# Kernel optimization log

Measured on AMD Instinct MI355X. Metric: run time of the kernel, lower is better.

## Reference

```python
import jax, jax.numpy as jnp
import numpy as np
import math

NUM_LANDMARKS = 64
HEAD_DIM = 64
NUM_HEAD = 16
BATCH = 4
SEQ_LEN = 4096


def iterative_inv(mat, n_iter=6):
    # mat: [..., m, m]
    I = jnp.eye(mat.shape[-1], dtype=mat.dtype)
    K = mat
    # scalar normalization: global max of column sums * global max of row sums
    scale = 1.0 / (jnp.max(jnp.sum(jnp.abs(K), axis=-2)) * jnp.max(jnp.sum(jnp.abs(K), axis=-1)))
    V = scale * jnp.swapaxes(K, -1, -2)
    for _ in range(n_iter):
        KV = jnp.matmul(K, V)
        V = jnp.matmul(0.25 * V, 13.0 * I - jnp.matmul(KV, 15.0 * I - jnp.matmul(KV, 7.0 * I - KV)))
    return V


def setup_inputs() -> dict:
    key = jax.random.key(0)
    k1, k2, k3 = jax.random.split(key, 3)
    shape = (BATCH, NUM_HEAD, SEQ_LEN, HEAD_DIM)
    Q = jax.random.normal(k1, shape, dtype=jnp.float32)
    K = jax.random.normal(k2, shape, dtype=jnp.float32)
    V = jax.random.normal(k3, shape, dtype=jnp.float32)
    return {"Q": Q, "K": K, "V": V}


def reference(Q, K, V):
    seq_len = Q.shape[-2]
    m = NUM_LANDMARKS
    scale = 1.0 / math.sqrt(math.sqrt(HEAD_DIM))
    Q = Q * scale
    K = K * scale
    # landmark pooling: mean over contiguous segments of length seq_len // m
    seg = seq_len // m
    Q_lm = Q.reshape(-1, NUM_HEAD, m, seg, HEAD_DIM).mean(axis=-2)  # [B,H,m,d]
    K_lm = K.reshape(-1, NUM_HEAD, m, seg, HEAD_DIM).mean(axis=-2)  # [B,H,m,d]
    # three softmax kernels
    kernel_1 = jax.nn.softmax(jnp.einsum('bhsd,bhmd->bhsm', Q, K_lm), axis=-1)   # [B,H,S,m]
    kernel_2 = jax.nn.softmax(jnp.einsum('bhmd,bhnd->bhmn', Q_lm, K_lm), axis=-1)  # [B,H,m,m]
    kernel_3 = jax.nn.softmax(jnp.einsum('bhmd,bhsd->bhms', Q_lm, K), axis=-1)   # [B,H,m,S]
    inv_k2 = iterative_inv(kernel_2)
    X = jnp.matmul(jnp.matmul(kernel_1, inv_k2), jnp.matmul(kernel_3, V))  # [B,H,S,d]
    return X
```

## Files before the change

### kernel.cpp

```cpp
#include <hip/hip_runtime.h>
#include <hip/hip_bf16.h>

#define PAD 68
#define KP  72
#define SCALE 0.35355339059327379f

typedef __attribute__((ext_vector_type(8))) short bf16x8;
typedef __attribute__((ext_vector_type(4))) float f32x4;
#define MFMA_BF16 __builtin_amdgcn_mfma_f32_16x16x32_bf16

__device__ __forceinline__ short f2b(float f) {
    unsigned u = __float_as_uint(f);
    u += 0x7fff + ((u >> 16) & 1);
    return (short)(u >> 16);
}
__device__ __forceinline__ float b2f(short h) {
    return __uint_as_float(((unsigned)(unsigned short)h) << 16);
}

__device__ __forceinline__ void fma16(float acc[16], float a, const float* b) {
    const float4* b4 = reinterpret_cast<const float4*>(b);
    float4 x0 = b4[0], x1 = b4[1], x2 = b4[2], x3 = b4[3];
    acc[0]  += a * x0.x; acc[1]  += a * x0.y; acc[2]  += a * x0.z; acc[3]  += a * x0.w;
    acc[4]  += a * x1.x; acc[5]  += a * x1.y; acc[6]  += a * x1.z; acc[7]  += a * x1.w;
    acc[8]  += a * x2.x; acc[9]  += a * x2.y; acc[10] += a * x2.z; acc[11] += a * x2.w;
    acc[12] += a * x3.x; acc[13] += a * x3.y; acc[14] += a * x3.z; acc[15] += a * x3.w;
}

__device__ __forceinline__ void mm_tile(float acc[4][4],
                                        const float* __restrict__ A, int lda,
                                        const float* __restrict__ B,
                                        int i0, int j0) {
#pragma unroll
    for (int r = 0; r < 4; r++)
#pragma unroll
        for (int c = 0; c < 4; c++) acc[r][c] = 0.f;
#pragma unroll 4
    for (int k0 = 0; k0 < 64; k0 += 4) {
        float4 b0 = *reinterpret_cast<const float4*>(&B[(k0 + 0) * PAD + j0]);
        float4 b1 = *reinterpret_cast<const float4*>(&B[(k0 + 1) * PAD + j0]);
        float4 b2 = *reinterpret_cast<const float4*>(&B[(k0 + 2) * PAD + j0]);
        float4 b3 = *reinterpret_cast<const float4*>(&B[(k0 + 3) * PAD + j0]);
        float4 a0 = *reinterpret_cast<const float4*>(&A[(i0 + 0) * lda + k0]);
        float4 a1 = *reinterpret_cast<const float4*>(&A[(i0 + 1) * lda + k0]);
        float4 a2 = *reinterpret_cast<const float4*>(&A[(i0 + 2) * lda + k0]);
        float4 a3 = *reinterpret_cast<const float4*>(&A[(i0 + 3) * lda + k0]);
#define ROW_UPD(r, av) \
        acc[r][0] += av.x * b0.x + av.y * b1.x + av.z * b2.x + av.w * b3.x; \
        acc[r][1] += av.x * b0.y + av.y * b1.y + av.z * b2.y + av.w * b3.y; \
        acc[r][2] += av.x * b0.z + av.y * b1.z + av.z * b2.z + av.w * b3.z; \
        acc[r][3] += av.x * b0.w + av.y * b1.w + av.z * b2.w + av.w * b3.w;
        ROW_UPD(0, a0) ROW_UPD(1, a1) ROW_UPD(2, a2) ROW_UPD(3, a3)
#undef ROW_UPD
    }
}

__global__ __launch_bounds__(256) void pool_kernel(const float* __restrict__ Q,
                                                   const float* __restrict__ K,
                                                   float* __restrict__ Qlm,
                                                   float* __restrict__ Klm) {
    __shared__ float4 red[256];
    const int blk = blockIdx.x;
    const int t = threadIdx.x;
    const int d4 = t & 15;
    const int rg = t >> 4;
    const float4* Q4 = reinterpret_cast<const float4*>(Q);
    const float4* K4 = reinterpret_cast<const float4*>(K);

    float4 sQ = {0.f, 0.f, 0.f, 0.f}, sK = {0.f, 0.f, 0.f, 0.f};
#pragma unroll
    for (int rr = 0; rr < 4; rr++) {
        int row = blk * 64 + rg * 4 + rr;
        int off4 = (row << 4) + d4;
        float4 q = Q4[off4], k = K4[off4];
        sQ.x += q.x; sQ.y += q.y; sQ.z += q.z; sQ.w += q.w;
        sK.x += k.x; sK.y += k.y; sK.z += k.z; sK.w += k.w;
    }
    const float c = SCALE * (1.0f / 64.0f);
    red[t] = sQ;
    __syncthreads();
    if (t < 16) {
        float4 s = {0.f, 0.f, 0.f, 0.f};
#pragma unroll
        for (int g = 0; g < 16; g++) {
            float4 v = red[g * 16 + t];
            s.x += v.x; s.y += v.y; s.z += v.z; s.w += v.w;
        }
        s.x *= c; s.y *= c; s.z *= c; s.w *= c;
        reinterpret_cast<float4*>(Qlm + blk * 64)[t] = s;
    }
    __syncthreads();
    red[t] = sK;
    __syncthreads();
    if (t < 16) {
        float4 s = {0.f, 0.f, 0.f, 0.f};
#pragma unroll
        for (int g = 0; g < 16; g++) {
            float4 v = red[g * 16 + t];
            s.x += v.x; s.y += v.y; s.z += v.z; s.w += v.w;
        }
        s.x *= c; s.y *= c; s.z *= c; s.w *= c;
        reinterpret_cast<float4*>(Klm + blk * 64)[t] = s;
    }
}

__global__ __launch_bounds__(256) void k2_kernel(const float* __restrict__ Qlm,
                                                 const float* __restrict__ Klm,
                                                 float* __restrict__ K2g,
                                                 unsigned* __restrict__ colmax) {
    __shared__ float Ql[64 * PAD], Kl[64 * PAD], S2[64 * PAD];
    const int bh = blockIdx.x, t = threadIdx.x;
#pragma unroll
    for (int n = 0; n < 16; n++) {
        int f = t + n * 256;
        Ql[(f >> 6) * PAD + (f & 63)] = Qlm[bh * 4096 + f];
        Kl[(f >> 6) * PAD + (f & 63)] = Klm[bh * 4096 + f];
    }
    __syncthreads();
    const int i = t >> 2, j0 = (t & 3) * 16;
    float acc[16];
#pragma unroll
    for (int u = 0; u < 16; u++) acc[u] = 0.f;
    const float4* Ql4 = reinterpret_cast<const float4*>(Ql);
    const float4* Kl4 = reinterpret_cast<const float4*>(Kl);
    for (int k4 = 0; k4 < 16; k4++) {
        float4 a = Ql4[i * 17 + k4];
#pragma unroll
        for (int u = 0; u < 16; u++) {
            float4 b = Kl4[(j0 + u) * 17 + k4];
            acc[u] += a.x * b.x + a.y * b.y + a.z * b.z + a.w * b.w;
        }
    }
#pragma unroll
    for (int u = 0; u < 16; u++) S2[i * PAD + j0 + u] = acc[u];
    __syncthreads();
    if (t < 64) {
        float m = -1e30f;
        for (int j = 0; j < 64; j++) m = fmaxf(m, S2[t * PAD + j]);
        float sum = 0.f;
        for (int j = 0; j < 64; j++) {
            float e = __expf(S2[t * PAD + j] - m);
            S2[t * PAD + j] = e; sum += e;
        }
        float inv = 1.0f / sum;
        for (int j = 0; j < 64; j++) S2[t * PAD + j] *= inv;
    }
    __syncthreads();
#pragma unroll
    for (int n = 0; n < 16; n++) {
        int f = t + n * 256;
        K2g[bh * 4096 + f] = S2[(f >> 6) * PAD + (f & 63)];
    }
    if (t < 64) {
        float c = 0.f;
        for (int ii = 0; ii < 64; ii++) c += S2[ii * PAD + t];
        atomicMax(colmax, __float_as_uint(c));
    }
}

__global__ __launch_bounds__(256) void fused_inv_k3v(const float* __restrict__ Qlm,
                                                     const float* __restrict__ K,
                                                     const float* __restrict__ V,
                                                     float* __restrict__ W2acc,
                                                     float* __restrict__ rowsum3,
                                                     const float* __restrict__ K2g,
                                                     const unsigned* __restrict__ colmax,
                                                     float* __restrict__ K2invg) {
    __shared__ __align__(16) char smem[64 * PAD * 4 * 3];
    const int t = threadIdx.x;

    if (blockIdx.x < 64) {
        float* Vb = reinterpret_cast<float*>(smem);
        float* Ab = Vb + 64 * PAD;
        float* Tb = Ab + 64 * PAD;
        const int bh = blockIdx.x;
        const float sc = 1.0f / __uint_as_float(*colmax);
        const float* Kg = K2g + bh * 4096;
#pragma unroll
        for (int n = 0; n < 16; n++) {
            int f = t + n * 256;
            Vb[(f >> 6) * PAD + (f & 63)] = sc * Kg[(f & 63) * 64 + (f >> 6)];
        }
        __syncthreads();
        const int i0 = (t >> 4) * 4, j0 = (t & 15) * 4;
        float acc[4][4], vacc[4][4];
        for (int iter = 0; iter < 6; iter++) {
            mm_tile(acc, Kg, 64, Vb, i0, j0);
#pragma unroll
            for (int r = 0; r < 4; r++)
                *reinterpret_cast<float4*>(&Ab[(i0 + r) * PAD + j0]) =
                    make_float4(acc[r][0], acc[r][1], acc[r][2], acc[r][3]);
            __syncthreads();
            mm_tile(acc, Vb, PAD, Ab, i0, j0);
#pragma unroll
            for (int r = 0; r < 4; r++) {
                float4 v = *reinterpret_cast<const float4*>(&Vb[(i0 + r) * PAD + j0]);
                vacc[r][0] = 13.f * v.x - 15.f * acc[r][0];
                vacc[r][1] = 13.f * v.y - 15.f * acc[r][1];
                vacc[r][2] = 13.f * v.z - 15.f * acc[r][2];
                vacc[r][3] = 13.f * v.w - 15.f * acc[r][3];
                *reinterpret_cast<float4*>(&Tb[(i0 + r) * PAD + j0]) =
                    make_float4(acc[r][0], acc[r][1], acc[r][2], acc[r][3]);
            }
            __syncthreads();
            mm_tile(acc, Tb, PAD, Ab, i0, j0);
#pragma unroll
            for (int r = 0; r < 4; r++) {
                vacc[r][0] += 7.f * acc[r][0];
                vacc[r][1] += 7.f * acc[r][1];
                vacc[r][2] += 7.f * acc[r][2];
                vacc[r][3] += 7.f * acc[r][3];
                *reinterpret_cast<float4*>(&Vb[(i0 + r) * PAD + j0]) =
                    make_float4(acc[r][0], acc[r][1], acc[r][2], acc[r][3]);
            }
            __syncthreads();
            mm_tile(acc, Vb, PAD, Ab, i0, j0);
#pragma unroll
            for (int r = 0; r < 4; r++) {
                vacc[r][0] -= acc[r][0]; vacc[r][1] -= acc[r][1];
                vacc[r][2] -= acc[r][2]; vacc[r][3] -= acc[r][3];
            }
            __syncthreads();
#pragma unroll
            for (int r = 0; r < 4; r++)
                *reinterpret_cast<float4*>(&Vb[(i0 + r) * PAD + j0]) =
                    make_float4(0.25f * vacc[r][0], 0.25f * vacc[r][1],
                                0.25f * vacc[r][2], 0.25f * vacc[r][3]);
            __syncthreads();
        }
#pragma unroll
        for (int n = 0; n < 16; n++) {
            int f = t + n * 256;
            K2invg[bh * 4096 + f] = Vb[(f >> 6) * PAD + (f & 63)];
        }
        return;
    }

    short* Qs = reinterpret_cast<short*>(smem);
    short* Kt = Qs + 64 * KP;
    short* Vt = Kt + 64 * KP;
    short* Eb = Vt + 64 * KP;
    const int idx = blockIdx.x - 64;
    const int chunk = idx & 15, bh = idx >> 4;
    const int w = t >> 6, lane = t & 63, quad = lane >> 4, l15 = lane & 15;
    const float4* Qlm4 = reinterpret_cast<const float4*>(Qlm);
    const float4* K4 = reinterpret_cast<const float4*>(K);
    const float4* V4 = reinterpret_cast<const float4*>(V);

#pragma unroll
    for (int n = 0; n < 4; n++) {
        int f4 = t + n * 256;
        int r = f4 >> 4, dg = f4 & 15;
        float4 q = Qlm4[bh * 1024 + f4];
        ushort4 uq = { (unsigned short)f2b(q.x), (unsigned short)f2b(q.y),
                       (unsigned short)f2b(q.z), (unsigned short)f2b(q.w) };
        *reinterpret_cast<ushort4*>(&Qs[r * KP + dg * 4]) = uq;
    }

    f32x4 oacc[4];
    float rsum[4];
#pragma unroll
    for (int nt = 0; nt < 4; nt++) { oacc[nt] = (f32x4){0.f, 0.f, 0.f, 0.f}; rsum[nt] = 0.f; }

    for (int tile = 0; tile < 4; tile++) {
        const int sb = chunk * 256 + tile * 64;
        __syncthreads();
#pragma unroll
        for (int n = 0; n < 4; n++) {
            int f4 = t + n * 256;
            int key = f4 >> 4, dg = f4 & 15;
            int g4 = (bh * 4096 + sb + key) * 16 + dg;
            float4 kk = K4[g4];
            ushort4 uk = { (unsigned short)f2b(SCALE * kk.x), (unsigned short)f2b(SCALE * kk.y),
                           (unsigned short)f2b(SCALE * kk.z), (unsigned short)f2b(SCALE * kk.w) };
            *reinterpret_cast<ushort4*>(&Kt[key * KP + dg * 4]) = uk;
            float4 vv = V4[g4];
            Vt[(dg * 4 + 0) * KP + key] = f2b(vv.x);
            Vt[(dg * 4 + 1) * KP + key] = f2b(vv.y);
            Vt[(dg * 4 + 2) * KP + key] = f2b(vv.z);
            Vt[(dg * 4 + 3) * KP + key] = f2b(vv.w);
        }
        __syncthreads();
        bf16x8 a0 = *reinterpret_cast<const bf16x8*>(&Qs[(w * 16 + l15) * KP + quad * 8]);
        bf16x8 a1 = *reinterpret_cast<const bf16x8*>(&Qs[(w * 16 + l15) * KP + quad * 8 + 32]);
#pragma unroll
        for (int nt = 0; nt < 4; nt++) {
            bf16x8 b0 = *reinterpret_cast<const bf16x8*>(&Kt[(nt * 16 + l15) * KP + quad * 8]);
            bf16x8 b1 = *reinterpret_cast<const bf16x8*>(&Kt[(nt * 16 + l15) * KP + quad * 8 + 32]);
            f32x4 c = {0.f, 0.f, 0.f, 0.f};
            c = MFMA_BF16(a0, b0, c, 0, 0, 0);
            c = MFMA_BF16(a1, b1, c, 0, 0, 0);
#pragma unroll
            for (int reg = 0; reg < 4; reg++) {
                float e = __expf(c[reg]);
                rsum[reg] += e;
                Eb[(w * 16 + quad * 4 + reg) * KP + nt * 16 + l15] = f2b(e);
            }
        }
        bf16x8 e0 = *reinterpret_cast<const bf16x8*>(&Eb[(w * 16 + l15) * KP + quad * 8]);
        bf16x8 e1 = *reinterpret_cast<const bf16x8*>(&Eb[(w * 16 + l15) * KP + quad * 8 + 32]);
#pragma unroll
        for (int nt = 0; nt < 4; nt++) {
            bf16x8 b0 = *reinterpret_cast<const bf16x8*>(&Vt[(nt * 16 + l15) * KP + quad * 8]);
            bf16x8 b1 = *reinterpret_cast<const bf16x8*>(&Vt[(nt * 16 + l15) * KP + quad * 8 + 32]);
            oacc[nt] = MFMA_BF16(e0, b0, oacc[nt], 0, 0, 0);
            oacc[nt] = MFMA_BF16(e1, b1, oacc[nt], 0, 0, 0);
        }
    }
#pragma unroll
    for (int reg = 0; reg < 4; reg++) {
        float s = rsum[reg];
        s += __shfl_xor(s, 1); s += __shfl_xor(s, 2);
        s += __shfl_xor(s, 4); s += __shfl_xor(s, 8);
        rsum[reg] = s;
    }
    const int row0 = w * 16 + quad * 4;
    if (l15 == 0) {
#pragma unroll
        for (int reg = 0; reg < 4; reg++)
            atomicAdd(&rowsum3[bh * 64 + row0 + reg], rsum[reg]);
    }
#pragma unroll
    for (int nt = 0; nt < 4; nt++)
#pragma unroll
        for (int reg = 0; reg < 4; reg++)
            atomicAdd(&W2acc[(bh * 64 + row0 + reg) * 64 + nt * 16 + l15], oacc[nt][reg]);
}

__global__ __launch_bounds__(256) void wmid_kernel(const float* __restrict__ K2invg,
                                                   const float* __restrict__ W2acc,
                                                   const float* __restrict__ rowsum3,
                                                   float* __restrict__ Wg) {
    __shared__ float I1[64 * PAD], W2[64 * PAD];
    const int bh = blockIdx.x, t = threadIdx.x;
#pragma unroll
    for (int n = 0; n < 16; n++) {
        int f = t + n * 256;
        int r = f >> 6;
        I1[r * PAD + (f & 63)] = K2invg[bh * 4096 + f];
        W2[r * PAD + (f & 63)] = W2acc[bh * 4096 + f] / rowsum3[bh * 64 + r];
    }
    __syncthreads();
    const int i = t >> 2, j0 = (t & 3) * 16;
    float acc[16];
#pragma unroll
    for (int u = 0; u < 16; u++) acc[u] = 0.f;
    for (int k = 0; k < 64; k++) fma16(acc, I1[i * PAD + k], W2 + k * PAD + j0);
#pragma unroll
    for (int u = 0; u < 16; u++) Wg[bh * 4096 + i * 64 + j0 + u] = acc[u];
}

__global__ __launch_bounds__(256) void final_mfma(const float* __restrict__ Q,
                                                  const float* __restrict__ Klm,
                                                  const float* __restrict__ Wg,
                                                  float* __restrict__ out) {
    __shared__ short Qs[64 * KP];
    __shared__ short Kl[64 * KP];
    __shared__ short Eb[64 * KP];
    __shared__ short Wh[64 * KP];
    __shared__ short Wl[64 * KP];
    const int sc = blockIdx.x, bh = blockIdx.y, t = threadIdx.x;
    const int w = t >> 6, lane = t & 63, quad = lane >> 4, l15 = lane & 15;
    const int s0 = sc * 64;
    const float4* Q4 = reinterpret_cast<const float4*>(Q);
    const float4* Klm4 = reinterpret_cast<const float4*>(Klm);
    const float4* W4 = reinterpret_cast<const float4*>(Wg);

#pragma unroll
    for (int n = 0; n < 4; n++) {
        int f4 = t + n * 256;
        int r = f4 >> 4, dg = f4 & 15;
        float4 kl = Klm4[bh * 1024 + f4];
        ushort4 uk = { (unsigned short)f2b(kl.x), (unsigned short)f2b(kl.y),
                       (unsigned short)f2b(kl.z), (unsigned short)f2b(kl.w) };
        *reinterpret_cast<ushort4*>(&Kl[r * KP + dg * 4]) = uk;
        float4 q = Q4[(bh * 4096 + s0 + r) * 16 + dg];
        ushort4 uq = { (unsigned short)f2b(SCALE * q.x), (unsigned short)f2b(SCALE * q.y),
                       (unsigned short)f2b(SCALE * q.z), (unsigned short)f2b(SCALE * q.w) };
        *reinterpret_cast<ushort4*>(&Qs[r * KP + dg * 4]) = uq;
        float4 ww = W4[bh * 1024 + f4];
        float wv[4] = {ww.x, ww.y, ww.z, ww.w};
#pragma unroll
        for (int i = 0; i < 4; i++) {
            short hi = f2b(wv[i]);
            Wh[(dg * 4 + i) * KP + r] = hi;
            Wl[(dg * 4 + i) * KP + r] = f2b(wv[i] - b2f(hi));
        }
    }
    __syncthreads();
    bf16x8 a0 = *reinterpret_cast<const bf16x8*>(&Qs[(w * 16 + l15) * KP + quad * 8]);
    bf16x8 a1 = *reinterpret_cast<const bf16x8*>(&Qs[(w * 16 + l15) * KP + quad * 8 + 32]);
    float rsum[4] = {0.f, 0.f, 0.f, 0.f};
#pragma unroll
    for (int nt = 0; nt < 4; nt++) {
        bf16x8 b0 = *reinterpret_cast<const bf16x8*>(&Kl[(nt * 16 + l15) * KP + quad * 8]);
        bf16x8 b1 = *reinterpret_cast<const bf16x8*>(&Kl[(nt * 16 + l15) * KP + quad * 8 + 32]);
        f32x4 c = {0.f, 0.f, 0.f, 0.f};
        c = MFMA_BF16(a0, b0, c, 0, 0, 0);
        c = MFMA_BF16(a1, b1, c, 0, 0, 0);
#pragma unroll
        for (int reg = 0; reg < 4; reg++) {
            float e = __expf(c[reg]);
            rsum[reg] += e;
            Eb[(w * 16 + quad * 4 + reg) * KP + nt * 16 + l15] = f2b(e);
        }
    }
#pragma unroll
    for (int reg = 0; reg < 4; reg++) {
        float s = rsum[reg];
        s += __shfl_xor(s, 1); s += __shfl_xor(s, 2);
        s += __shfl_xor(s, 4); s += __shfl_xor(s, 8);
        rsum[reg] = 1.0f / s;
    }
    bf16x8 e0 = *reinterpret_cast<const bf16x8*>(&Eb[(w * 16 + l15) * KP + quad * 8]);
    bf16x8 e1 = *reinterpret_cast<const bf16x8*>(&Eb[(w * 16 + l15) * KP + quad * 8 + 32]);
    const int row0 = w * 16 + quad * 4;
#pragma unroll
    for (int nt = 0; nt < 4; nt++) {
        bf16x8 bh0 = *reinterpret_cast<const bf16x8*>(&Wh[(nt * 16 + l15) * KP + quad * 8]);
        bf16x8 bh1 = *reinterpret_cast<const bf16x8*>(&Wh[(nt * 16 + l15) * KP + quad * 8 + 32]);
        bf16x8 bl0 = *reinterpret_cast<const bf16x8*>(&Wl[(nt * 16 + l15) * KP + quad * 8]);
        bf16x8 bl1 = *reinterpret_cast<const bf16x8*>(&Wl[(nt * 16 + l15) * KP + quad * 8 + 32]);
        f32x4 c = {0.f, 0.f, 0.f, 0.f};
        c = MFMA_BF16(e0, bh0, c, 0, 0, 0);
        c = MFMA_BF16(e1, bh1, c, 0, 0, 0);
        c = MFMA_BF16(e0, bl0, c, 0, 0, 0);
        c = MFMA_BF16(e1, bl1, c, 0, 0, 0);
#pragma unroll
        for (int reg = 0; reg < 4; reg++)
            out[((size_t)bh * 4096 + s0 + row0 + reg) * 64 + nt * 16 + l15] = c[reg] * rsum[reg];
    }
}

extern "C" void kernel_launch(void* const* d_in, const int* in_sizes, int n_in,
                              void* d_out, int out_size, void* d_ws, size_t ws_size,
                              hipStream_t stream) {
    const float* Q = (const float*)d_in[0];
    const float* K = (const float*)d_in[1];
    const float* V = (const float*)d_in[2];
    float* out = (float*)d_out;
    float* ws = (float*)d_ws;

    float* Qlm    = ws;
    float* Klm    = ws + 262144;
    float* K2     = ws + 524288;
    float* K2inv  = ws + 786432;
    float* Wg     = ws + 1048576;
    float* W2acc  = ws + 1310720;
    float* rowsum3 = ws + 1572864;
    unsigned* colmax = (unsigned*)(ws + 1576960);

    hipMemsetAsync(W2acc, 0, (262144 + 4096 + 1) * sizeof(float), stream);

    pool_kernel<<<4096, 256, 0, stream>>>(Q, K, Qlm, Klm);
    k2_kernel<<<64, 256, 0, stream>>>(Qlm, Klm, K2, colmax);
    fused_inv_k3v<<<1088, 256, 0, stream>>>(Qlm, K, V, W2acc, rowsum3, K2, colmax, K2inv);
    wmid_kernel<<<64, 256, 0, stream>>>(K2inv, W2acc, rowsum3, Wg);
    final_mfma<<<dim3(64, 64), 256, 0, stream>>>(Q, Klm, Wg, out);
}
```

Before: 310.3 us.

## Prefetch K/V and Q tiles into registers and enlarge per-block work

In the fused K3·V kernel each block now processes 512 keys instead of 256, and the next tile's K and V loads are issued into registers before the current tile is computed. V's transpose into LDS now uses vectorized ushort4 stores from a remapped thread-to-key assignment. final_mfma loops over four 64-row Q tiles per block with register prefetch, so the Klm and W staging (including the hi/lo split of W) is amortized over four tiles. Both grids shrink by the same factors, cutting block setup overhead and hiding global load latency, at the cost of fewer blocks in flight, more registers per thread, and an occupancy hint of 3 on the fused kernel.

```diff
diff --git a/kernel.cpp b/kernel.cpp
--- a/kernel.cpp
+++ b/kernel.cpp
@@ -158,14 +158,14 @@
     }
 }
 
-__global__ __launch_bounds__(256) void fused_inv_k3v(const float* __restrict__ Qlm,
-                                                     const float* __restrict__ K,
-                                                     const float* __restrict__ V,
-                                                     float* __restrict__ W2acc,
-                                                     float* __restrict__ rowsum3,
-                                                     const float* __restrict__ K2g,
-                                                     const unsigned* __restrict__ colmax,
-                                                     float* __restrict__ K2invg) {
+__global__ __launch_bounds__(256, 3) void fused_inv_k3v(const float* __restrict__ Qlm,
+                                                        const float* __restrict__ K,
+                                                        const float* __restrict__ V,
+                                                        float* __restrict__ W2acc,
+                                                        float* __restrict__ rowsum3,
+                                                        const float* __restrict__ K2g,
+                                                        const unsigned* __restrict__ colmax,
+                                                        float* __restrict__ K2invg) {
     __shared__ __align__(16) char smem[64 * PAD * 4 * 3];
     const int t = threadIdx.x;
 
@@ -241,20 +241,23 @@
     short* Vt = Kt + 64 * KP;
     short* Eb = Vt + 64 * KP;
     const int idx = blockIdx.x - 64;
-    const int chunk = idx & 15, bh = idx >> 4;
+    const int chunk = idx & 7, bh = idx >> 3;
     const int w = t >> 6, lane = t & 63, quad = lane >> 4, l15 = lane & 15;
     const float4* Qlm4 = reinterpret_cast<const float4*>(Qlm);
     const float4* K4 = reinterpret_cast<const float4*>(K);
     const float4* V4 = reinterpret_cast<const float4*>(V);
+    const int dg = t & 15;
+    const int kr = t >> 4;
+    const int bhBase = bh * 4096;
 
 #pragma unroll
     for (int n = 0; n < 4; n++) {
         int f4 = t + n * 256;
-        int r = f4 >> 4, dg = f4 & 15;
+        int r = f4 >> 4, dgq = f4 & 15;
         float4 q = Qlm4[bh * 1024 + f4];
         ushort4 uq = { (unsigned short)f2b(q.x), (unsigned short)f2b(q.y),
                        (unsigned short)f2b(q.z), (unsigned short)f2b(q.w) };
-        *reinterpret_cast<ushort4*>(&Qs[r * KP + dg * 4]) = uq;
+        *reinterpret_cast<ushort4*>(&Qs[r * KP + dgq * 4]) = uq;
     }
 
     f32x4 oacc[4];
@@ -262,23 +265,48 @@
 #pragma unroll
     for (int nt = 0; nt < 4; nt++) { oacc[nt] = (f32x4){0.f, 0.f, 0.f, 0.f}; rsum[nt] = 0.f; }
 
-    for (int tile = 0; tile < 4; tile++) {
-        const int sb = chunk * 256 + tile * 64;
+    const int sb0 = chunk * 512;
+    float4 pk0 = K4[(bhBase + sb0 + kr +  0) * 16 + dg];
+    float4 pk1 = K4[(bhBase + sb0 + kr + 16) * 16 + dg];
+    float4 pk2 = K4[(bhBase + sb0 + kr + 32) * 16 + dg];
+    float4 pk3 = K4[(bhBase + sb0 + kr + 48) * 16 + dg];
+    float4 pv0 = V4[(bhBase + sb0 + kr * 4 + 0) * 16 + dg];
+    float4 pv1 = V4[(bhBase + sb0 + kr * 4 + 1) * 16 + dg];
+    float4 pv2 = V4[(bhBase + sb0 + kr * 4 + 2) * 16 + dg];
+    float4 pv3 = V4[(bhBase + sb0 + kr * 4 + 3) * 16 + dg];
+
+    for (int tile = 0; tile < 8; tile++) {
         __syncthreads();
-#pragma unroll
-        for (int n = 0; n < 4; n++) {
-            int f4 = t + n * 256;
-            int key = f4 >> 4, dg = f4 & 15;
-            int g4 = (bh * 4096 + sb + key) * 16 + dg;
-            float4 kk = K4[g4];
-            ushort4 uk = { (unsigned short)f2b(SCALE * kk.x), (unsigned short)f2b(SCALE * kk.y),
-                           (unsigned short)f2b(SCALE * kk.z), (unsigned short)f2b(SCALE * kk.w) };
-            *reinterpret_cast<ushort4*>(&Kt[key * KP + dg * 4]) = uk;
-            float4 vv = V4[g4];
-            Vt[(dg * 4 + 0) * KP + key] = f2b(vv.x);
-            Vt[(dg * 4 + 1) * KP + key] = f2b(vv.y);
-            Vt[(dg * 4 + 2) * KP + key] = f2b(vv.z);
-            Vt[(dg * 4 + 3) * KP + key] = f2b(vv.w);
+#define KWRITE(n, pk) { \
+        ushort4 uk = { (unsigned short)f2b(SCALE * pk.x), (unsigned short)f2b(SCALE * pk.y), \
+                       (unsigned short)f2b(SCALE * pk.z), (unsigned short)f2b(SCALE * pk.w) }; \
+        *reinterpret_cast<ushort4*>(&Kt[(kr + 16 * n) * KP + dg * 4]) = uk; }
+        KWRITE(0, pk0) KWRITE(1, pk1) KWRITE(2, pk2) KWRITE(3, pk3)
+#undef KWRITE
+        {
+            ushort4 u0 = { (unsigned short)f2b(pv0.x), (unsigned short)f2b(pv1.x),
+                           (unsigned short)f2b(pv2.x), (unsigned short)f2b(pv3.x) };
+            ushort4 u1 = { (unsigned short)f2b(pv0.y), (unsigned short)f2b(pv1.y),
+                           (unsigned short)f2b(pv2.y), (unsigned short)f2b(pv3.y) };
+            ushort4 u2 = { (unsigned short)f2b(pv0.z), (unsigned short)f2b(pv1.z),
+                           (unsigned short)f2b(pv2.z), (unsigned short)f2b(pv3.z) };
+            ushort4 u3 = { (unsigned short)f2b(pv0.w), (unsigned short)f2b(pv1.w),
+                           (unsigned short)f2b(pv2.w), (unsigned short)f2b(pv3.w) };
+            *reinterpret_cast<ushort4*>(&Vt[(dg * 4 + 0) * KP + kr * 4]) = u0;
+            *reinterpret_cast<ushort4*>(&Vt[(dg * 4 + 1) * KP + kr * 4]) = u1;
+            *reinterpret_cast<ushort4*>(&Vt[(dg * 4 + 2) * KP + kr * 4]) = u2;
+            *reinterpret_cast<ushort4*>(&Vt[(dg * 4 + 3) * KP + kr * 4]) = u3;
+        }
+        if (tile < 7) {
+            const int sb = sb0 + (tile + 1) * 64;
+            pk0 = K4[(bhBase + sb + kr +  0) * 16 + dg];
+            pk1 = K4[(bhBase + sb + kr + 16) * 16 + dg];
+            pk2 = K4[(bhBase + sb + kr + 32) * 16 + dg];
+            pk3 = K4[(bhBase + sb + kr + 48) * 16 + dg];
+            pv0 = V4[(bhBase + sb + kr * 4 + 0) * 16 + dg];
+            pv1 = V4[(bhBase + sb + kr * 4 + 1) * 16 + dg];
+            pv2 = V4[(bhBase + sb + kr * 4 + 2) * 16 + dg];
+            pv3 = V4[(bhBase + sb + kr * 4 + 3) * 16 + dg];
         }
         __syncthreads();
         bf16x8 a0 = *reinterpret_cast<const bf16x8*>(&Qs[(w * 16 + l15) * KP + quad * 8]);
@@ -361,7 +389,8 @@
     __shared__ short Wl[64 * KP];
     const int sc = blockIdx.x, bh = blockIdx.y, t = threadIdx.x;
     const int w = t >> 6, lane = t & 63, quad = lane >> 4, l15 = lane & 15;
-    const int s0 = sc * 64;
+    const int s0 = sc * 256;
+    const int rr = t >> 4, dg = t & 15;
     const float4* Q4 = reinterpret_cast<const float4*>(Q);
     const float4* Klm4 = reinterpret_cast<const float4*>(Klm);
     const float4* W4 = reinterpret_cast<const float4*>(Wg);
@@ -369,66 +398,84 @@
 #pragma unroll
     for (int n = 0; n < 4; n++) {
         int f4 = t + n * 256;
-        int r = f4 >> 4, dg = f4 & 15;
+        int r = f4 >> 4, dgq = f4 & 15;
         float4 kl = Klm4[bh * 1024 + f4];
         ushort4 uk = { (unsigned short)f2b(kl.x), (unsigned short)f2b(kl.y),
                        (unsigned short)f2b(kl.z), (unsigned short)f2b(kl.w) };
-        *reinterpret_cast<ushort4*>(&Kl[r * KP + dg * 4]) = uk;
-        float4 q = Q4[(bh * 4096 + s0 + r) * 16 + dg];
-        ushort4 uq = { (unsigned short)f2b(SCALE * q.x), (unsigned short)f2b(SCALE * q.y),
-                       (unsigned short)f2b(SCALE * q.z), (unsigned short)f2b(SCALE * q.w) };
-        *reinterpret_cast<ushort4*>(&Qs[r * KP + dg * 4]) = uq;
+        *reinterpret_cast<ushort4*>(&Kl[r * KP + dgq * 4]) = uk;
         float4 ww = W4[bh * 1024 + f4];
         float wv[4] = {ww.x, ww.y, ww.z, ww.w};
 #pragma unroll
         for (int i = 0; i < 4; i++) {
             short hi = f2b(wv[i]);
-            Wh[(dg * 4 + i) * KP + r] = hi;
-            Wl[(dg * 4 + i) * KP + r] = f2b(wv[i] - b2f(hi));
-        }
-    }
-    __syncthreads();
-    bf16x8 a0 = *reinterpret_cast<const bf16x8*>(&Qs[(w * 16 + l15) * KP + quad * 8]);
-    bf16x8 a1 = *reinterpret_cast<const bf16x8*>(&Qs[(w * 16 + l15) * KP + quad * 8 + 32]);
-    float rsum[4] = {0.f, 0.f, 0.f, 0.f};
-#pragma unroll
-    for (int nt = 0; nt < 4; nt++) {
-        bf16x8 b0 = *reinterpret_cast<const bf16x8*>(&Kl[(nt * 16 + l15) * KP + quad * 8]);
-        bf16x8 b1 = *reinterpret_cast<const bf16x8*>(&Kl[(nt * 16 + l15) * KP + quad * 8 + 32]);
-        f32x4 c = {0.f, 0.f, 0.f, 0.f};
-        c = MFMA_BF16(a0, b0, c, 0, 0, 0);
-        c = MFMA_BF16(a1, b1, c, 0, 0, 0);
+            Wh[(dgq * 4 + i) * KP + r] = hi;
+            Wl[(dgq * 4 + i) * KP + r] = f2b(wv[i] - b2f(hi));
+        }
+    }
+    float4 q0 = Q4[(bh * 4096 + s0 + rr +  0) * 16 + dg];
+    float4 q1 = Q4[(bh * 4096 + s0 + rr + 16) * 16 + dg];
+    float4 q2 = Q4[(bh * 4096 + s0 + rr + 32) * 16 + dg];
+    float4 q3 = Q4[(bh * 4096 + s0 + rr + 48) * 16 + dg];
+
+    for (int st = 0; st < 4; st++) {
+        __syncthreads();
+#define QWRITE(n, qv) { \
+        ushort4 uq = { (unsigned short)f2b(SCALE * qv.x), (unsigned short)f2b(SCALE * qv.y), \
+                       (unsigned short)f2b(SCALE * qv.z), (unsigned short)f2b(SCALE * qv.w) }; \
+        *reinterpret_cast<ushort4*>(&Qs[(rr + 16 * n) * KP + dg * 4]) = uq; }
+        QWRITE(0, q0) QWRITE(1, q1) QWRITE(2, q2) QWRITE(3, q3)
+#undef QWRITE
+        if (st < 3) {
+            const int sq = s0 + (st + 1) * 64;
+            q0 = Q4[(bh * 4096 + sq + rr +  0) * 16 + dg];
+            q1 = Q4[(bh * 4096 + sq + rr + 16) * 16 + dg];
+            q2 = Q4[(bh * 4096 + sq + rr + 32) * 16 + dg];
+            q3 = Q4[(bh * 4096 + sq + rr + 48) * 16 + dg];
+        }
+        __syncthreads();
+        bf16x8 a0 = *reinterpret_cast<const bf16x8*>(&Qs[(w * 16 + l15) * KP + quad * 8]);
+        bf16x8 a1 = *reinterpret_cast<const bf16x8*>(&Qs[(w * 16 + l15) * KP + quad * 8 + 32]);
+        float rsum[4] = {0.f, 0.f, 0.f, 0.f};
+#pragma unroll
+        for (int nt = 0; nt < 4; nt++) {
+            bf16x8 b0 = *reinterpret_cast<const bf16x8*>(&Kl[(nt * 16 + l15) * KP + quad * 8]);
+            bf16x8 b1 = *reinterpret_cast<const bf16x8*>(&Kl[(nt * 16 + l15) * KP + quad * 8 + 32]);
+            f32x4 c = {0.f, 0.f, 0.f, 0.f};
+            c = MFMA_BF16(a0, b0, c, 0, 0, 0);
+            c = MFMA_BF16(a1, b1, c, 0, 0, 0);
+#pragma unroll
+            for (int reg = 0; reg < 4; reg++) {
+                float e = __expf(c[reg]);
+                rsum[reg] += e;
+                Eb[(w * 16 + quad * 4 + reg) * KP + nt * 16 + l15] = f2b(e);
+            }
+        }
 #pragma unroll
         for (int reg = 0; reg < 4; reg++) {
-            float e = __expf(c[reg]);
-            rsum[reg] += e;
-            Eb[(w * 16 + quad * 4 + reg) * KP + nt * 16 + l15] = f2b(e);
-        }
-    }
-#pragma unroll
-    for (int reg = 0; reg < 4; reg++) {
-        float s = rsum[reg];
-        s += __shfl_xor(s, 1); s += __shfl_xor(s, 2);
-        s += __shfl_xor(s, 4); s += __shfl_xor(s, 8);
-        rsum[reg] = 1.0f / s;
-    }
-    bf16x8 e0 = *reinterpret_cast<const bf16x8*>(&Eb[(w * 16 + l15) * KP + quad * 8]);
-    bf16x8 e1 = *reinterpret_cast<const bf16x8*>(&Eb[(w * 16 + l15) * KP + quad * 8 + 32]);
-    const int row0 = w * 16 + quad * 4;
-#pragma unroll
-    for (int nt = 0; nt < 4; nt++) {
-        bf16x8 bh0 = *reinterpret_cast<const bf16x8*>(&Wh[(nt * 16 + l15) * KP + quad * 8]);
-        bf16x8 bh1 = *reinterpret_cast<const bf16x8*>(&Wh[(nt * 16 + l15) * KP + quad * 8 + 32]);
-        bf16x8 bl0 = *reinterpret_cast<const bf16x8*>(&Wl[(nt * 16 + l15) * KP + quad * 8]);
-        bf16x8 bl1 = *reinterpret_cast<const bf16x8*>(&Wl[(nt * 16 + l15) * KP + quad * 8 + 32]);
-        f32x4 c = {0.f, 0.f, 0.f, 0.f};
-        c = MFMA_BF16(e0, bh0, c, 0, 0, 0);
-        c = MFMA_BF16(e1, bh1, c, 0, 0, 0);
-        c = MFMA_BF16(e0, bl0, c, 0, 0, 0);
-        c = MFMA_BF16(e1, bl1, c, 0, 0, 0);
-#pragma unroll
-        for (int reg = 0; reg < 4; reg++)
-            out[((size_t)bh * 4096 + s0 + row0 + reg) * 64 + nt * 16 + l15] = c[reg] * rsum[reg];
+            float s = rsum[reg];
+            s += __shfl_xor(s, 1); s += __shfl_xor(s, 2);
+            s += __shfl_xor(s, 4); s += __shfl_xor(s, 8);
+            rsum[reg] = 1.0f / s;
+        }
+        bf16x8 e0 = *reinterpret_cast<const bf16x8*>(&Eb[(w * 16 + l15) * KP + quad * 8]);
+        bf16x8 e1 = *reinterpret_cast<const bf16x8*>(&Eb[(w * 16 + l15) * KP + quad * 8 + 32]);
+        const int row0 = w * 16 + quad * 4;
+#pragma unroll
+        for (int nt = 0; nt < 4; nt++) {
+            bf16x8 bh0 = *reinterpret_cast<const bf16x8*>(&Wh[(nt * 16 + l15) * KP + quad * 8]);
+            bf16x8 bh1 = *reinterpret_cast<const bf16x8*>(&Wh[(nt * 16 + l15) * KP + quad * 8 + 32]);
+            bf16x8 bl0 = *reinterpret_cast<const bf16x8*>(&Wl[(nt * 16 + l15) * KP + quad * 8]);
+            bf16x8 bl1 = *reinterpret_cast<const bf16x8*>(&Wl[(nt * 16 + l15) * KP + quad * 8 + 32]);
+            f32x4 c = {0.f, 0.f, 0.f, 0.f};
+            c = MFMA_BF16(e0, bh0, c, 0, 0, 0);
+            c = MFMA_BF16(e1, bh1, c, 0, 0, 0);
+            c = MFMA_BF16(e0, bl0, c, 0, 0, 0);
+            c = MFMA_BF16(e1, bl1, c, 0, 0, 0);
+#pragma unroll
+            for (int reg = 0; reg < 4; reg++)
+                out[((size_t)bh * 4096 + s0 + st * 64 + row0 + reg) * 64 + nt * 16 + l15] =
+                    c[reg] * rsum[reg];
+        }
     }
 }
 
@@ -454,7 +501,7 @@
 
     pool_kernel<<<4096, 256, 0, stream>>>(Q, K, Qlm, Klm);
     k2_kernel<<<64, 256, 0, stream>>>(Qlm, Klm, K2, colmax);
-    fused_inv_k3v<<<1088, 256, 0, stream>>>(Qlm, K, V, W2acc, rowsum3, K2, colmax, K2inv);
+    fused_inv_k3v<<<576, 256, 0, stream>>>(Qlm, K, V, W2acc, rowsum3, K2, colmax, K2inv);
     wmid_kernel<<<64, 256, 0, stream>>>(K2inv, W2acc, rowsum3, Wg);
-    final_mfma<<<dim3(64, 64), 256, 0, stream>>>(Q, Klm, Wg, out);
-}
+    final_mfma<<<dim3(16, 64), 256, 0, stream>>>(Q, Klm, Wg, out);
+}
```

Result: slower. 325.1 us (+4.8%).

## Precompute bf16 landmarks and transposed W split, load MFMA operands directly from global

Applied to the files above, without the earlier changes.

The pool kernel now also writes bf16 copies of the landmark Q/K, and wmid writes W pre-split into hi/lo bf16 in transposed layout. This lets the k3v and final kernels load MFMA operands straight from global memory instead of converting and staging them in shared memory, which removes LDS traffic and a barrier in the final kernel. The k3v phase doubles its block count so each block handles two tiles instead of four, and V transposition is done with packed 4-wide stores. The cost is extra workspace writes and uncoalesced-ish global vector loads per lane, plus more atomics into W2acc from the extra blocks.

```diff
diff --git a/kernel.cpp b/kernel.cpp
--- a/kernel.cpp
+++ b/kernel.cpp
@@ -58,7 +58,9 @@
 __global__ __launch_bounds__(256) void pool_kernel(const float* __restrict__ Q,
                                                    const float* __restrict__ K,
                                                    float* __restrict__ Qlm,
-                                                   float* __restrict__ Klm) {
+                                                   float* __restrict__ Klm,
+                                                   short* __restrict__ Qlm_b,
+                                                   short* __restrict__ Klm_b) {
     __shared__ float4 red[256];
     const int blk = blockIdx.x;
     const int t = threadIdx.x;
@@ -88,6 +90,9 @@
         }
         s.x *= c; s.y *= c; s.z *= c; s.w *= c;
         reinterpret_cast<float4*>(Qlm + blk * 64)[t] = s;
+        ushort4 ub = { (unsigned short)f2b(s.x), (unsigned short)f2b(s.y),
+                       (unsigned short)f2b(s.z), (unsigned short)f2b(s.w) };
+        *reinterpret_cast<ushort4*>(&Qlm_b[blk * 64 + t * 4]) = ub;
     }
     __syncthreads();
     red[t] = sK;
@@ -101,6 +106,9 @@
         }
         s.x *= c; s.y *= c; s.z *= c; s.w *= c;
         reinterpret_cast<float4*>(Klm + blk * 64)[t] = s;
+        ushort4 ub = { (unsigned short)f2b(s.x), (unsigned short)f2b(s.y),
+                       (unsigned short)f2b(s.z), (unsigned short)f2b(s.w) };
+        *reinterpret_cast<ushort4*>(&Klm_b[blk * 64 + t * 4]) = ub;
     }
 }
 
@@ -158,7 +166,7 @@
     }
 }
 
-__global__ __launch_bounds__(256) void fused_inv_k3v(const float* __restrict__ Qlm,
+__global__ __launch_bounds__(256) void fused_inv_k3v(const short* __restrict__ Qlm_b,
                                                      const float* __restrict__ K,
                                                      const float* __restrict__ V,
                                                      float* __restrict__ W2acc,
@@ -236,53 +244,57 @@
         return;
     }
 
-    short* Qs = reinterpret_cast<short*>(smem);
-    short* Kt = Qs + 64 * KP;
+    short* Kt = reinterpret_cast<short*>(smem);
     short* Vt = Kt + 64 * KP;
     short* Eb = Vt + 64 * KP;
     const int idx = blockIdx.x - 64;
-    const int chunk = idx & 15, bh = idx >> 4;
+    const int chunk = idx & 31, bh = idx >> 5;
     const int w = t >> 6, lane = t & 63, quad = lane >> 4, l15 = lane & 15;
-    const float4* Qlm4 = reinterpret_cast<const float4*>(Qlm);
     const float4* K4 = reinterpret_cast<const float4*>(K);
     const float4* V4 = reinterpret_cast<const float4*>(V);
-
-#pragma unroll
-    for (int n = 0; n < 4; n++) {
-        int f4 = t + n * 256;
-        int r = f4 >> 4, dg = f4 & 15;
-        float4 q = Qlm4[bh * 1024 + f4];
-        ushort4 uq = { (unsigned short)f2b(q.x), (unsigned short)f2b(q.y),
-                       (unsigned short)f2b(q.z), (unsigned short)f2b(q.w) };
-        *reinterpret_cast<ushort4*>(&Qs[r * KP + dg * 4]) = uq;
-    }
+    const int dg = t & 15;
+    const int kr = t >> 4;
+    const int bhBase = bh * 4096;
+
+    const bf16x8* Qb = reinterpret_cast<const bf16x8*>(Qlm_b + bh * 4096);
+    bf16x8 a0 = Qb[(w * 16 + l15) * 8 + quad];
+    bf16x8 a1 = Qb[(w * 16 + l15) * 8 + quad + 4];
 
     f32x4 oacc[4];
     float rsum[4];
 #pragma unroll
     for (int nt = 0; nt < 4; nt++) { oacc[nt] = (f32x4){0.f, 0.f, 0.f, 0.f}; rsum[nt] = 0.f; }
 
-    for (int tile = 0; tile < 4; tile++) {
-        const int sb = chunk * 256 + tile * 64;
+    const int sb0 = chunk * 128;
+    for (int tile = 0; tile < 2; tile++) {
+        const int sb = sb0 + tile * 64;
         __syncthreads();
 #pragma unroll
         for (int n = 0; n < 4; n++) {
-            int f4 = t + n * 256;
-            int key = f4 >> 4, dg = f4 & 15;
-            int g4 = (bh * 4096 + sb + key) * 16 + dg;
-            float4 kk = K4[g4];
+            float4 kk = K4[(bhBase + sb + kr + 16 * n) * 16 + dg];
             ushort4 uk = { (unsigned short)f2b(SCALE * kk.x), (unsigned short)f2b(SCALE * kk.y),
                            (unsigned short)f2b(SCALE * kk.z), (unsigned short)f2b(SCALE * kk.w) };
-            *reinterpret_cast<ushort4*>(&Kt[key * KP + dg * 4]) = uk;
-            float4 vv = V4[g4];
-            Vt[(dg * 4 + 0) * KP + key] = f2b(vv.x);
-            Vt[(dg * 4 + 1) * KP + key] = f2b(vv.y);
-            Vt[(dg * 4 + 2) * KP + key] = f2b(vv.z);
-            Vt[(dg * 4 + 3) * KP + key] = f2b(vv.w);
+            *reinterpret_cast<ushort4*>(&Kt[(kr + 16 * n) * KP + dg * 4]) = uk;
+        }
+        {
+            float4 pv0 = V4[(bhBase + sb + kr * 4 + 0) * 16 + dg];
+            float4 pv1 = V4[(bhBase + sb + kr * 4 + 1) * 16 + dg];
+            float4 pv2 = V4[(bhBase + sb + kr * 4 + 2) * 16 + dg];
+            float4 pv3 = V4[(bhBase + sb + kr * 4 + 3) * 16 + dg];
+            ushort4 u0 = { (unsigned short)f2b(pv0.x), (unsigned short)f2b(pv1.x),
+                           (unsigned short)f2b(pv2.x), (unsigned short)f2b(pv3.x) };
+            ushort4 u1 = { (unsigned short)f2b(pv0.y), (unsigned short)f2b(pv1.y),
+                           (unsigned short)f2b(pv2.y), (unsigned short)f2b(pv3.y) };
+            ushort4 u2 = { (unsigned short)f2b(pv0.z), (unsigned short)f2b(pv1.z),
+                           (unsigned short)f2b(pv2.z), (unsigned short)f2b(pv3.z) };
+            ushort4 u3 = { (unsigned short)f2b(pv0.w), (unsigned short)f2b(pv1.w),
+                           (unsigned short)f2b(pv2.w), (unsigned short)f2b(pv3.w) };
+            *reinterpret_cast<ushort4*>(&Vt[(dg * 4 + 0) * KP + kr * 4]) = u0;
+            *reinterpret_cast<ushort4*>(&Vt[(dg * 4 + 1) * KP + kr * 4]) = u1;
+            *reinterpret_cast<ushort4*>(&Vt[(dg * 4 + 2) * KP + kr * 4]) = u2;
+            *reinterpret_cast<ushort4*>(&Vt[(dg * 4 + 3) * KP + kr * 4]) = u3;
         }
         __syncthreads();
-        bf16x8 a0 = *reinterpret_cast<const bf16x8*>(&Qs[(w * 16 + l15) * KP + quad * 8]);
-        bf16x8 a1 = *reinterpret_cast<const bf16x8*>(&Qs[(w * 16 + l15) * KP + quad * 8 + 32]);
 #pragma unroll
         for (int nt = 0; nt < 4; nt++) {
             bf16x8 b0 = *reinterpret_cast<const bf16x8*>(&Kt[(nt * 16 + l15) * KP + quad * 8]);
@@ -330,7 +342,8 @@
 __global__ __launch_bounds__(256) void wmid_kernel(const float* __restrict__ K2invg,
                                                    const float* __restrict__ W2acc,
                                                    const float* __restrict__ rowsum3,
-                                                   float* __restrict__ Wg) {
+                                                   short* __restrict__ Wth,
+                                                   short* __restrict__ Wtl) {
     __shared__ float I1[64 * PAD], W2[64 * PAD];
     const int bh = blockIdx.x, t = threadIdx.x;
 #pragma unroll
@@ -347,54 +360,51 @@
     for (int u = 0; u < 16; u++) acc[u] = 0.f;
     for (int k = 0; k < 64; k++) fma16(acc, I1[i * PAD + k], W2 + k * PAD + j0);
 #pragma unroll
-    for (int u = 0; u < 16; u++) Wg[bh * 4096 + i * 64 + j0 + u] = acc[u];
+    for (int u = 0; u < 16; u++) {
+        float wv = acc[u];
+        short hi = f2b(wv);
+        short lo = f2b(wv - b2f(hi));
+        Wth[bh * 4096 + (j0 + u) * 64 + i] = hi;
+        Wtl[bh * 4096 + (j0 + u) * 64 + i] = lo;
+    }
 }
 
 __global__ __launch_bounds__(256) void final_mfma(const float* __restrict__ Q,
-                                                  const float* __restrict__ Klm,
-                                                  const float* __restrict__ Wg,
+                                                  const short* __restrict__ Klm_b,
+                                                  const short* __restrict__ Wth,
+                                                  const short* __restrict__ Wtl,
                                                   float* __restrict__ out) {
-    __shared__ short Qs[64 * KP];
-    __shared__ short Kl[64 * KP];
     __shared__ short Eb[64 * KP];
-    __shared__ short Wh[64 * KP];
-    __shared__ short Wl[64 * KP];
     const int sc = blockIdx.x, bh = blockIdx.y, t = threadIdx.x;
     const int w = t >> 6, lane = t & 63, quad = lane >> 4, l15 = lane & 15;
     const int s0 = sc * 64;
-    const float4* Q4 = reinterpret_cast<const float4*>(Q);
-    const float4* Klm4 = reinterpret_cast<const float4*>(Klm);
-    const float4* W4 = reinterpret_cast<const float4*>(Wg);
-
-#pragma unroll
-    for (int n = 0; n < 4; n++) {
-        int f4 = t + n * 256;
-        int r = f4 >> 4, dg = f4 & 15;
-        float4 kl = Klm4[bh * 1024 + f4];
-        ushort4 uk = { (unsigned short)f2b(kl.x), (unsigned short)f2b(kl.y),
-                       (unsigned short)f2b(kl.z), (unsigned short)f2b(kl.w) };
-        *reinterpret_cast<ushort4*>(&Kl[r * KP + dg * 4]) = uk;
-        float4 q = Q4[(bh * 4096 + s0 + r) * 16 + dg];
-        ushort4 uq = { (unsigned short)f2b(SCALE * q.x), (unsigned short)f2b(SCALE * q.y),
-                       (unsigned short)f2b(SCALE * q.z), (unsigned short)f2b(SCALE * q.w) };
-        *reinterpret_cast<ushort4*>(&Qs[r * KP + dg * 4]) = uq;
-        float4 ww = W4[bh * 1024 + f4];
-        float wv[4] = {ww.x, ww.y, ww.z, ww.w};
-#pragma unroll
-        for (int i = 0; i < 4; i++) {
-            short hi = f2b(wv[i]);
-            Wh[(dg * 4 + i) * KP + r] = hi;
-            Wl[(dg * 4 + i) * KP + r] = f2b(wv[i] - b2f(hi));
-        }
-    }
-    __syncthreads();
-    bf16x8 a0 = *reinterpret_cast<const bf16x8*>(&Qs[(w * 16 + l15) * KP + quad * 8]);
-    bf16x8 a1 = *reinterpret_cast<const bf16x8*>(&Qs[(w * 16 + l15) * KP + quad * 8 + 32]);
+    const int row = w * 16 + l15;
+
+    const float* qrow = Q + ((size_t)bh * 4096 + s0 + row) * 64 + quad * 8;
+    float4 qa = *reinterpret_cast<const float4*>(qrow);
+    float4 qb = *reinterpret_cast<const float4*>(qrow + 4);
+    float4 qc = *reinterpret_cast<const float4*>(qrow + 32);
+    float4 qd = *reinterpret_cast<const float4*>(qrow + 36);
+
+    const bf16x8* Kb = reinterpret_cast<const bf16x8*>(Klm_b + bh * 4096);
+    const bf16x8* Hb = reinterpret_cast<const bf16x8*>(Wth + bh * 4096);
+    const bf16x8* Lb = reinterpret_cast<const bf16x8*>(Wtl + bh * 4096);
+
+    bf16x8 a0, a1;
+    a0[0] = f2b(SCALE * qa.x); a0[1] = f2b(SCALE * qa.y);
+    a0[2] = f2b(SCALE * qa.z); a0[3] = f2b(SCALE * qa.w);
+    a0[4] = f2b(SCALE * qb.x); a0[5] = f2b(SCALE * qb.y);
+    a0[6] = f2b(SCALE * qb.z); a0[7] = f2b(SCALE * qb.w);
+    a1[0] = f2b(SCALE * qc.x); a1[1] = f2b(SCALE * qc.y);
+    a1[2] = f2b(SCALE * qc.z); a1[3] = f2b(SCALE * qc.w);
+    a1[4] = f2b(SCALE * qd.x); a1[5] = f2b(SCALE * qd.y);
+    a1[6] = f2b(SCALE * qd.z); a1[7] = f2b(SCALE * qd.w);
+
     float rsum[4] = {0.f, 0.f, 0.f, 0.f};
 #pragma unroll
     for (int nt = 0; nt < 4; nt++) {
-        bf16x8 b0 = *reinterpret_cast<const bf16x8*>(&Kl[(nt * 16 + l15) * KP + quad * 8]);
-        bf16x8 b1 = *reinterpret_cast<const bf16x8*>(&Kl[(nt * 16 + l15) * KP + quad * 8 + 32]);
+        bf16x8 b0 = Kb[(nt * 16 + l15) * 8 + quad];
+        bf16x8 b1 = Kb[(nt * 16 + l15) * 8 + quad + 4];
         f32x4 c = {0.f, 0.f, 0.f, 0.f};
         c = MFMA_BF16(a0, b0, c, 0, 0, 0);
         c = MFMA_BF16(a1, b1, c, 0, 0, 0);
@@ -412,15 +422,15 @@
         s += __shfl_xor(s, 4); s += __shfl_xor(s, 8);
         rsum[reg] = 1.0f / s;
     }
-    bf16x8 e0 = *reinterpret_cast<const bf16x8*>(&Eb[(w * 16 + l15) * KP + quad * 8]);
-    bf16x8 e1 = *reinterpret_cast<const bf16x8*>(&Eb[(w * 16 + l15) * KP + quad * 8 + 32]);
+    bf16x8 e0 = *reinterpret_cast<const bf16x8*>(&Eb[row * KP + quad * 8]);
+    bf16x8 e1 = *reinterpret_cast<const bf16x8*>(&Eb[row * KP + quad * 8 + 32]);
     const int row0 = w * 16 + quad * 4;
 #pragma unroll
     for (int nt = 0; nt < 4; nt++) {
-        bf16x8 bh0 = *reinterpret_cast<const bf16x8*>(&Wh[(nt * 16 + l15) * KP + quad * 8]);
-        bf16x8 bh1 = *reinterpret_cast<const bf16x8*>(&Wh[(nt * 16 + l15) * KP + quad * 8 + 32]);
-        bf16x8 bl0 = *reinterpret_cast<const bf16x8*>(&Wl[(nt * 16 + l15) * KP + quad * 8]);
-        bf16x8 bl1 = *reinterpret_cast<const bf16x8*>(&Wl[(nt * 16 + l15) * KP + quad * 8 + 32]);
+        bf16x8 bh0 = Hb[(nt * 16 + l15) * 8 + quad];
+        bf16x8 bh1 = Hb[(nt * 16 + l15) * 8 + quad + 4];
+        bf16x8 bl0 = Lb[(nt * 16 + l15) * 8 + quad];
+        bf16x8 bl1 = Lb[(nt * 16 + l15) * 8 + quad + 4];
         f32x4 c = {0.f, 0.f, 0.f, 0.f};
         c = MFMA_BF16(e0, bh0, c, 0, 0, 0);
         c = MFMA_BF16(e1, bh1, c, 0, 0, 0);
@@ -441,20 +451,23 @@
     float* out = (float*)d_out;
     float* ws = (float*)d_ws;
 
-    float* Qlm    = ws;
-    float* Klm    = ws + 262144;
-    float* K2     = ws + 524288;
-    float* K2inv  = ws + 786432;
-    float* Wg     = ws + 1048576;
-    float* W2acc  = ws + 1310720;
+    float* Qlm     = ws;
+    float* Klm     = ws + 262144;
+    float* K2      = ws + 524288;
+    float* K2inv   = ws + 786432;
+    short* Wth     = (short*)(ws + 1048576);
+    short* Wtl     = (short*)(ws + 1179648);
+    float* W2acc   = ws + 1310720;
     float* rowsum3 = ws + 1572864;
     unsigned* colmax = (unsigned*)(ws + 1576960);
+    short* Qlm_b   = (short*)(ws + 1576964);
+    short* Klm_b   = (short*)(ws + 1708036);
 
     hipMemsetAsync(W2acc, 0, (262144 + 4096 + 1) * sizeof(float), stream);
 
-    pool_kernel<<<4096, 256, 0, stream>>>(Q, K, Qlm, Klm);
+    pool_kernel<<<4096, 256, 0, stream>>>(Q, K, Qlm, Klm, Qlm_b, Klm_b);
     k2_kernel<<<64, 256, 0, stream>>>(Qlm, Klm, K2, colmax);
-    fused_inv_k3v<<<1088, 256, 0, stream>>>(Qlm, K, V, W2acc, rowsum3, K2, colmax, K2inv);
-    wmid_kernel<<<64, 256, 0, stream>>>(K2inv, W2acc, rowsum3, Wg);
-    final_mfma<<<dim3(64, 64), 256, 0, stream>>>(Q, Klm, Wg, out);
-}
+    fused_inv_k3v<<<2112, 256, 0, stream>>>(Qlm_b, K, V, W2acc, rowsum3, K2, colmax, K2inv);
+    wmid_kernel<<<64, 256, 0, stream>>>(K2inv, W2acc, rowsum3, Wth, Wtl);
+    final_mfma<<<dim3(64, 64), 256, 0, stream>>>(Q, Klm_b, Wth, Wtl, out);
+}
```

Result: slower. 337.6 us (+8.8%).
